# Kernel tuning notes

Measured on AMD Instinct MI355X. Metric: run time of the kernel, lower is better.

The kernel has to match this reference:

```python
import jax, jax.numpy as jnp
import numpy as np

B, S, D = 16, 2048, 1024   # batch, src_len, per-tensor feature dim (input_dim*growth_factor)
OUT = 1024                 # output_dim


def setup_inputs() -> dict:
    key = jax.random.key(0)
    k1, k2, k3, k4, k5, k6 = jax.random.split(key, 6)
    hidden = jax.random.normal(k1, (B, S, D), dtype=jnp.float32)
    encoder_outputs = jax.random.normal(k2, (B, S, D), dtype=jnp.float32)
    c_t = jax.random.normal(k3, (B, D), dtype=jnp.float32)
    # Linear(input_dim*3*growth_factor=3*D, OUT): PyTorch stores weight as [OUT, 3D]
    limit = 1.0 / np.sqrt(3 * D)
    W = jax.random.uniform(k4, (OUT, 3 * D), minval=-limit, maxval=limit, dtype=jnp.float32)
    b = jax.random.uniform(k5, (OUT,), minval=-limit, maxval=limit, dtype=jnp.float32)
    v = jax.random.uniform(k6, (OUT,), dtype=jnp.float32)  # torch.rand -> U[0,1)
    return {"hidden": hidden, "encoder_outputs": encoder_outputs, "c_t": c_t,
            "W": W, "b": b, "v": v}


def reference(hidden, encoder_outputs, c_t, W, b, v):
    # c_t broadcast over src_len; concat on feature dim -> [B, S, 3D]
    c_rep = jnp.broadcast_to(c_t[:, None, :], hidden.shape)
    cat = jnp.concatenate((hidden, c_rep, encoder_outputs), axis=2)
    # energy = relu(cat @ W^T + b): [B, S, OUT]
    energy = jax.nn.relu(jnp.einsum('bsf,of->bso', cat, W) + b)
    # attention = energy @ v: [B, S], then softmax over src_len
    attention = jnp.einsum('bso,o->bs', energy, v)
    return jax.nn.softmax(attention, axis=1)
```

## Files before the change

kernel.cpp:

```cpp
#include <hip/hip_runtime.h>
#include <hip/hip_bf16.h>


typedef __attribute__((ext_vector_type(8))) short short8;
typedef __attribute__((ext_vector_type(4))) float f32x4;
typedef __attribute__((ext_vector_type(8))) unsigned short ushort8v;
typedef __attribute__((ext_vector_type(4))) unsigned short ushort4v;

#define NB 16
#define NS 2048
#define ND 1024
#define NOUT 1024
#define NM (NB * NS)
#define KHE 2048
#define TM 256
#define TN 128
#define BK 64
#define NROWS (TM + TN)

#define PREP_ACONV 16384
#define PREP_WCONV 2048
#define PREP_CBIAS 256
#define PREP_ZERO 32

__device__ __forceinline__ unsigned short bf16_rne(float x) {
    unsigned int u = __float_as_uint(x);
    unsigned int r = (u + 0x7fffu + ((u >> 16) & 1u)) >> 16;
    return (unsigned short)r;
}

__device__ __forceinline__ void gload_lds16(const unsigned short* g, unsigned short* l) {
    __builtin_amdgcn_global_load_lds(
        (const __attribute__((address_space(1))) void*)g,
        (__attribute__((address_space(3))) void*)l, 16, 0, 0);
}

__global__ __launch_bounds__(256) void prep_k(const float* __restrict__ hidden,
                                              const float* __restrict__ enc,
                                              const float* __restrict__ c_t,
                                              const float* __restrict__ W,
                                              const float* __restrict__ bias,
                                              unsigned short* __restrict__ Abf,
                                              unsigned short* __restrict__ Wbf,
                                              float* __restrict__ cbias,
                                              float* __restrict__ logits) {
    const int bid = blockIdx.x;
    const int tid = threadIdx.x;
    if (bid < PREP_ACONV) {
        size_t c = (size_t)bid * 256 + tid;
        size_t m = c >> 7;
        int k = (int)(c & 127) * 16;
        const float* src = (k < ND) ? (hidden + m * ND + k) : (enc + m * ND + (k - ND));
        float4 f0 = ((const float4*)src)[0];
        float4 f1 = ((const float4*)src)[1];
        float4 f2 = ((const float4*)src)[2];
        float4 f3 = ((const float4*)src)[3];
        ushort8v h0, h1;
        h0[0] = bf16_rne(f0.x); h0[1] = bf16_rne(f0.y); h0[2] = bf16_rne(f0.z); h0[3] = bf16_rne(f0.w);
        h0[4] = bf16_rne(f1.x); h0[5] = bf16_rne(f1.y); h0[6] = bf16_rne(f1.z); h0[7] = bf16_rne(f1.w);
        h1[0] = bf16_rne(f2.x); h1[1] = bf16_rne(f2.y); h1[2] = bf16_rne(f2.z); h1[3] = bf16_rne(f2.w);
        h1[4] = bf16_rne(f3.x); h1[5] = bf16_rne(f3.y); h1[6] = bf16_rne(f3.z); h1[7] = bf16_rne(f3.w);
        *(ushort8v*)(Abf + m * KHE + k) = h0;
        *(ushort8v*)(Abf + m * KHE + k + 8) = h1;
    } else if (bid < PREP_ACONV + PREP_WCONV) {
        int idx = (bid - PREP_ACONV) * 256 + tid;
        int o = idx >> 9;
        int k = (idx & 511) * 4;
        int off = (k < ND) ? k : (k + ND);
        float4 f = *(const float4*)(W + (size_t)o * 3072 + off);
        ushort4v h;
        h.x = bf16_rne(f.x); h.y = bf16_rne(f.y); h.z = bf16_rne(f.z); h.w = bf16_rne(f.w);
        *(ushort4v*)(Wbf + (size_t)o * KHE + k) = h;
    } else if (bid < PREP_ACONV + PREP_WCONV + PREP_CBIAS) {
        int o = (bid - PREP_ACONV - PREP_WCONV) * 4 + (tid >> 6);
        int lane = tid & 63;
        const float* w = W + (size_t)o * 3072 + ND;
        float wr[16];
        #pragma unroll
        for (int j = 0; j < 16; ++j) wr[j] = w[lane + j * 64];
        float bo = bias[o];
        for (int b = 0; b < NB; ++b) {
            const float* cc = c_t + (size_t)b * ND;
            float s = 0.f;
            #pragma unroll
            for (int j = 0; j < 16; ++j) s = fmaf(cc[lane + j * 64], wr[j], s);
            #pragma unroll
            for (int m = 1; m < 64; m <<= 1) s += __shfl_xor(s, m);
            if (lane == 0) cbias[b * NOUT + o] = s + bo;
        }
    } else {
        int idx = (bid - PREP_ACONV - PREP_WCONV - PREP_CBIAS) * 256 + tid;
        ((float4*)logits)[idx] = make_float4(0.f, 0.f, 0.f, 0.f);
    }
}

__global__ __launch_bounds__(256) void wconv_k(const float* __restrict__ W,
                                               unsigned short* __restrict__ Wbf) {
    int idx = blockIdx.x * 256 + threadIdx.x;
    int o = idx >> 9;
    int k = (idx & 511) * 4;
    int off = (k < ND) ? k : (k + ND);
    float4 f = *(const float4*)(W + (size_t)o * 3072 + off);
    ushort4v h;
    h.x = bf16_rne(f.x); h.y = bf16_rne(f.y); h.z = bf16_rne(f.z); h.w = bf16_rne(f.w);
    *(ushort4v*)(Wbf + (size_t)o * KHE + k) = h;
}

__global__ __launch_bounds__(256) void cbias_k(const float* __restrict__ c_t,
                                               const float* __restrict__ W,
                                               const float* __restrict__ bias,
                                               float* __restrict__ cbias) {
    int o = blockIdx.x * 4 + (threadIdx.x >> 6);
    int lane = threadIdx.x & 63;
    const float* w = W + (size_t)o * 3072 + ND;
    float wr[16];
    #pragma unroll
    for (int j = 0; j < 16; ++j) wr[j] = w[lane + j * 64];
    float bo = bias[o];
    for (int b = 0; b < NB; ++b) {
        const float* c = c_t + (size_t)b * ND;
        float s = 0.f;
        #pragma unroll
        for (int j = 0; j < 16; ++j) s = fmaf(c[lane + j * 64], wr[j], s);
        #pragma unroll
        for (int m = 1; m < 64; m <<= 1) s += __shfl_xor(s, m);
        if (lane == 0) cbias[b * NOUT + o] = s + bo;
    }
}

__global__ __launch_bounds__(512, 4) void gemm_att_bf_k(const unsigned short* __restrict__ Abf,
                                                        const unsigned short* __restrict__ Wbf,
                                                        const float* __restrict__ cbias,
                                                        const float* __restrict__ v,
                                                        float* __restrict__ logits) {
    __shared__ unsigned short Ls[NROWS * BK] __attribute__((aligned(16)));
    __shared__ float rowsum[2][TM];
    __shared__ float cb_s[TN];
    __shared__ float v_s[TN];

    const int tid = threadIdx.x;
    const int bid = blockIdx.x;
    const int ntile = bid & 7;
    const int mtile = bid >> 3;
    const int m0 = mtile * TM;
    const int o0 = ntile * TN;
    const int batch = m0 >> 11;

    if (tid < TN) {
        cb_s[tid] = cbias[batch * NOUT + o0 + tid];
        v_s[tid] = v[o0 + tid];
    }

    const int wid = tid >> 6;
    const int lane = tid & 63;
    const int wm = (wid & 3) * 64;
    const int wn = (wid >> 2) * 64;

    const int srow = lane >> 3;
    const int schunk = (lane & 7) ^ srow;

    f32x4 acc[4][4] = {};

    for (int kt = 0; kt < KHE; kt += BK) {
        #pragma unroll
        for (int t = 0; t < 6; ++t) {
            const int r0 = wid * 48 + t * 8;
            const unsigned short* src = (r0 < TM)
                ? (Abf + (size_t)(m0 + r0 + srow) * KHE + kt + schunk * 8)
                : (Wbf + (size_t)(o0 + r0 - TM + srow) * KHE + kt + schunk * 8);
            gload_lds16(src, Ls + r0 * BK);
        }
        __syncthreads();

        #pragma unroll
        for (int s = 0; s < 2; ++s) {
            const int cbase = s * 4 + (lane >> 4);
            short8 a_frag[4], b_frag[4];
            #pragma unroll
            for (int i = 0; i < 4; ++i) {
                int row = wm + i * 16 + (lane & 15);
                a_frag[i] = *(const short8*)(Ls + row * BK + ((cbase ^ (row & 7)) * 8));
            }
            #pragma unroll
            for (int j = 0; j < 4; ++j) {
                int row = TM + wn + j * 16 + (lane & 15);
                b_frag[j] = *(const short8*)(Ls + row * BK + ((cbase ^ (row & 7)) * 8));
            }
            #pragma unroll
            for (int i = 0; i < 4; ++i)
                #pragma unroll
                for (int j = 0; j < 4; ++j)
                    acc[i][j] = __builtin_amdgcn_mfma_f32_16x16x32_bf16(a_frag[i], b_frag[j],
                                                                        acc[i][j], 0, 0, 0);
        }
        __syncthreads();
    }

    const int col = lane & 15;
    const int q = lane >> 4;
    float vv[4], cbv[4];
    #pragma unroll
    for (int j = 0; j < 4; ++j) {
        int oc = wn + j * 16 + col;
        vv[j] = v_s[oc];
        cbv[j] = cb_s[oc];
    }
    #pragma unroll
    for (int i = 0; i < 4; ++i) {
        #pragma unroll
        for (int r = 0; r < 4; ++r) {
            float s = 0.f;
            #pragma unroll
            for (int j = 0; j < 4; ++j) {
                float e = acc[i][j][r] + cbv[j];
                e = fmaxf(e, 0.f);
                s = fmaf(e, vv[j], s);
            }
            s += __shfl_xor(s, 1);
            s += __shfl_xor(s, 2);
            s += __shfl_xor(s, 4);
            s += __shfl_xor(s, 8);
            if (col == 0) rowsum[wid >> 2][wm + i * 16 + q * 4 + r] = s;
        }
    }
    __syncthreads();
    if (tid < TM) atomicAdd(&logits[m0 + tid], rowsum[0][tid] + rowsum[1][tid]);
}

__global__ __launch_bounds__(256) void gemm_att_k(const float* __restrict__ hidden,
                                                  const float* __restrict__ enc,
                                                  const unsigned short* __restrict__ Wbf,
                                                  const float* __restrict__ Wf,
                                                  const float* __restrict__ cbias,
                                                  const float* __restrict__ v,
                                                  float* __restrict__ logits,
                                                  int use_wbf) {
    __shared__ unsigned short As[128 * 32] __attribute__((aligned(16)));
    __shared__ unsigned short Bs[128 * 32] __attribute__((aligned(16)));
    __shared__ float rowsum[2][128];
    __shared__ float cb_s[128];
    __shared__ float v_s[128];

    const int tid = threadIdx.x;
    const int ntile = blockIdx.x & 7;
    const int mtile = blockIdx.x >> 3;
    const int m0 = mtile * 128;
    const int o0 = ntile * 128;
    const int batch = m0 >> 11;

    if (tid < 128) {
        cb_s[tid] = cbias[batch * NOUT + o0 + tid];
        v_s[tid] = v[o0 + tid];
    }

    const int wid = tid >> 6;
    const int lane = tid & 63;
    const int wm = (wid & 1) * 64;
    const int wn = (wid >> 1) * 64;

    f32x4 acc[4][4] = {};

    for (int kt = 0; kt < KHE; kt += 32) {
        const float* Abase = (kt < ND) ? hidden : enc;
        const int aoff = (kt < ND) ? kt : (kt - ND);
        #pragma unroll
        for (int i = 0; i < 4; ++i) {
            int p = tid + i * 256;
            int row = p >> 3, kc = p & 7;
            float4 f = *(const float4*)(Abase + (size_t)(m0 + row) * ND + aoff + kc * 4);
            ushort4v h;
            h.x = bf16_rne(f.x); h.y = bf16_rne(f.y); h.z = bf16_rne(f.z); h.w = bf16_rne(f.w);
            *(ushort4v*)(As + row * 32 + kc * 4) = h;
        }
        if (use_wbf) {
            #pragma unroll
            for (int i = 0; i < 2; ++i) {
                int u = tid + i * 256;
                int ol = u >> 2, kc = u & 3;
                ushort8v w8 = *(const ushort8v*)(Wbf + (size_t)(o0 + ol) * KHE + kt + kc * 8);
                *(ushort8v*)(Bs + ol * 32 + kc * 8) = w8;
            }
        } else {
            const int woff = (kt < ND) ? kt : (kt + ND);
            #pragma unroll
            for (int i = 0; i < 4; ++i) {
                int p = tid + i * 256;
                int row = p >> 3, kc = p & 7;
                float4 f = *(const float4*)(Wf + (size_t)(o0 + row) * 3072 + woff + kc * 4);
                ushort4v h;
                h.x = bf16_rne(f.x); h.y = bf16_rne(f.y); h.z = bf16_rne(f.z); h.w = bf16_rne(f.w);
                *(ushort4v*)(Bs + row * 32 + kc * 4) = h;
            }
        }
        __syncthreads();

        short8 a_frag[4], b_frag[4];
        #pragma unroll
        for (int i = 0; i < 4; ++i)
            a_frag[i] = *(const short8*)(As + (wm + i * 16 + (lane & 15)) * 32 + (lane >> 4) * 8);
        #pragma unroll
        for (int j = 0; j < 4; ++j)
            b_frag[j] = *(const short8*)(Bs + (wn + j * 16 + (lane & 15)) * 32 + (lane >> 4) * 8);
        #pragma unroll
        for (int i = 0; i < 4; ++i)
            #pragma unroll
            for (int j = 0; j < 4; ++j)
                acc[i][j] = __builtin_amdgcn_mfma_f32_16x16x32_bf16(a_frag[i], b_frag[j],
                                                                    acc[i][j], 0, 0, 0);
        __syncthreads();
    }

    const int col = lane & 15;
    const int q = lane >> 4;
    float vv[4], cbv[4];
    #pragma unroll
    for (int j = 0; j < 4; ++j) {
        int oc = wn + j * 16 + col;
        vv[j] = v_s[oc];
        cbv[j] = cb_s[oc];
    }
    #pragma unroll
    for (int i = 0; i < 4; ++i) {
        #pragma unroll
        for (int r = 0; r < 4; ++r) {
            float s = 0.f;
            #pragma unroll
            for (int j = 0; j < 4; ++j) {
                float e = acc[i][j][r] + cbv[j];
                e = fmaxf(e, 0.f);
                s = fmaf(e, vv[j], s);
            }
            s += __shfl_xor(s, 1);
            s += __shfl_xor(s, 2);
            s += __shfl_xor(s, 4);
            s += __shfl_xor(s, 8);
            if (col == 0) rowsum[wid >> 1][wm + i * 16 + q * 4 + r] = s;
        }
    }
    __syncthreads();
    if (tid < 128) atomicAdd(&logits[m0 + tid], rowsum[0][tid] + rowsum[1][tid]);
}

__global__ __launch_bounds__(256) void softmax_k(const float* __restrict__ logits,
                                                 float* __restrict__ out) {
    const int b = blockIdx.x;
    const int tid = threadIdx.x;
    const int lane = tid & 63, wid = tid >> 6;
    __shared__ float redmax[4];
    __shared__ float redsum[4];
    const float* L = logits + (size_t)b * NS;
    float x[8];
    float mx = -3.4e38f;
    #pragma unroll
    for (int i = 0; i < 8; ++i) {
        x[i] = L[tid + i * 256];
        mx = fmaxf(mx, x[i]);
    }
    #pragma unroll
    for (int m = 1; m < 64; m <<= 1) mx = fmaxf(mx, __shfl_xor(mx, m));
    if (lane == 0) redmax[wid] = mx;
    __syncthreads();
    mx = fmaxf(fmaxf(redmax[0], redmax[1]), fmaxf(redmax[2], redmax[3]));
    float sum = 0.f;
    #pragma unroll
    for (int i = 0; i < 8; ++i) {
        x[i] = expf(x[i] - mx);
        sum += x[i];
    }
    #pragma unroll
    for (int m = 1; m < 64; m <<= 1) sum += __shfl_xor(sum, m);
    if (lane == 0) redsum[wid] = sum;
    __syncthreads();
    float inv = 1.0f / (redsum[0] + redsum[1] + redsum[2] + redsum[3]);
    #pragma unroll
    for (int i = 0; i < 8; ++i) out[(size_t)b * NS + tid + i * 256] = x[i] * inv;
}

extern "C" void kernel_launch(void* const* d_in, const int* in_sizes, int n_in,
                              void* d_out, int out_size, void* d_ws, size_t ws_size,
                              hipStream_t stream) {
    const float* hidden = (const float*)d_in[0];
    const float* enc    = (const float*)d_in[1];
    const float* c_t    = (const float*)d_in[2];
    const float* W      = (const float*)d_in[3];
    const float* bias   = (const float*)d_in[4];
    const float* v      = (const float*)d_in[5];
    float* out = (float*)d_out;

    char* ws = (char*)d_ws;
    float* logits = (float*)ws;
    float* cbias  = (float*)(ws + 131072);
    unsigned short* Wbf = (unsigned short*)(ws + 196608);
    unsigned short* Abf = (unsigned short*)(ws + 196608 + 4194304);
    const size_t need_wbf = 196608 + (size_t)NOUT * KHE * 2;
    const size_t need_abf = need_wbf + (size_t)NM * KHE * 2;

    if (ws_size >= need_abf) {
        prep_k<<<PREP_ACONV + PREP_WCONV + PREP_CBIAS + PREP_ZERO, 256, 0, stream>>>(
            hidden, enc, c_t, W, bias, Abf, Wbf, cbias, logits);
        gemm_att_bf_k<<<(NM / TM) * (NOUT / TN), 512, 0, stream>>>(Abf, Wbf, cbias, v, logits);
    } else if (ws_size >= need_wbf) {
        hipMemsetAsync(logits, 0, NM * sizeof(float), stream);
        cbias_k<<<NOUT / 4, 256, 0, stream>>>(c_t, W, bias, cbias);
        wconv_k<<<(NOUT * KHE / 4) / 256, 256, 0, stream>>>(W, Wbf);
        gemm_att_k<<<(NM / 128) * (NOUT / 128), 256, 0, stream>>>(hidden, enc, Wbf, W, cbias, v,
                                                                  logits, 1);
    } else {
        hipMemsetAsync(logits, 0, NM * sizeof(float), stream);
        cbias_k<<<NOUT / 4, 256, 0, stream>>>(c_t, W, bias, cbias);
        gemm_att_k<<<(NM / 128) * (NOUT / 128), 256, 0, stream>>>(hidden, enc, Wbf, W, cbias, v,
                                                                  logits, 0);
    }
    softmax_k<<<NB, 256, 0, stream>>>(logits, out);
}
```

Before: 457.2 us.

## Fuse bf16 conversion, GEMM-attention and softmax into one persistent kernel

Replaces the prep kernel, the GEMM kernel and the softmax kernel with a single 512-block kernel. Each block converts its own slice of A to bf16, and the first 64 blocks also convert W and compute the context bias. Blocks then spin on global atomic counters before running two N-tiles of the MFMA GEMM, and the first 16 blocks wait for all blocks to finish before computing the softmax. This removes launch gaps and lets conversion overlap with compute. The cost is inter-block spin waits that assume all 512 blocks are co-resident, which risks deadlock if they are not, plus a reduced grid with more serial work per block.

```diff
diff --git a/kernel.cpp b/kernel.cpp
--- a/kernel.cpp
+++ b/kernel.cpp
@@ -18,11 +18,6 @@
 #define BK 64
 #define NROWS (TM + TN)
 
-#define PREP_ACONV 16384
-#define PREP_WCONV 2048
-#define PREP_CBIAS 256
-#define PREP_ZERO 32
-
 __device__ __forceinline__ unsigned short bf16_rne(float x) {
     unsigned int u = __float_as_uint(x);
     unsigned int r = (u + 0x7fffu + ((u >> 16) & 1u)) >> 16;
@@ -35,63 +30,232 @@
         (__attribute__((address_space(3))) void*)l, 16, 0, 0);
 }
 
-__global__ __launch_bounds__(256) void prep_k(const float* __restrict__ hidden,
-                                              const float* __restrict__ enc,
-                                              const float* __restrict__ c_t,
-                                              const float* __restrict__ W,
-                                              const float* __restrict__ bias,
-                                              unsigned short* __restrict__ Abf,
-                                              unsigned short* __restrict__ Wbf,
-                                              float* __restrict__ cbias,
-                                              float* __restrict__ logits) {
+__device__ __forceinline__ void cvt16(const float* src, unsigned short* dst) {
+    float4 f0 = ((const float4*)src)[0];
+    float4 f1 = ((const float4*)src)[1];
+    float4 f2 = ((const float4*)src)[2];
+    float4 f3 = ((const float4*)src)[3];
+    ushort8v h0, h1;
+    h0[0] = bf16_rne(f0.x); h0[1] = bf16_rne(f0.y); h0[2] = bf16_rne(f0.z); h0[3] = bf16_rne(f0.w);
+    h0[4] = bf16_rne(f1.x); h0[5] = bf16_rne(f1.y); h0[6] = bf16_rne(f1.z); h0[7] = bf16_rne(f1.w);
+    h1[0] = bf16_rne(f2.x); h1[1] = bf16_rne(f2.y); h1[2] = bf16_rne(f2.z); h1[3] = bf16_rne(f2.w);
+    h1[4] = bf16_rne(f3.x); h1[5] = bf16_rne(f3.y); h1[6] = bf16_rne(f3.z); h1[7] = bf16_rne(f3.w);
+    *(ushort8v*)dst = h0;
+    *(ushort8v*)(dst + 8) = h1;
+}
+
+__global__ __launch_bounds__(512, 4) void fused_k(const float* __restrict__ hidden,
+                                                  const float* __restrict__ enc,
+                                                  const float* __restrict__ c_t,
+                                                  const float* __restrict__ W,
+                                                  const float* __restrict__ bias,
+                                                  const float* __restrict__ v,
+                                                  unsigned int* __restrict__ ctr,
+                                                  unsigned short* __restrict__ Abf,
+                                                  unsigned short* __restrict__ Wbf,
+                                                  float* __restrict__ cbias,
+                                                  float* __restrict__ logits,
+                                                  float* __restrict__ out) {
+    __shared__ unsigned short Ls[NROWS * BK] __attribute__((aligned(16)));
+    __shared__ float rowsum[2][TM];
+    __shared__ float cb_s[TN];
+    __shared__ float v_s[TN];
+
+    const int tid = threadIdx.x;
     const int bid = blockIdx.x;
-    const int tid = threadIdx.x;
-    if (bid < PREP_ACONV) {
-        size_t c = (size_t)bid * 256 + tid;
-        size_t m = c >> 7;
-        int k = (int)(c & 127) * 16;
-        const float* src = (k < ND) ? (hidden + m * ND + k) : (enc + m * ND + (k - ND));
-        float4 f0 = ((const float4*)src)[0];
-        float4 f1 = ((const float4*)src)[1];
-        float4 f2 = ((const float4*)src)[2];
-        float4 f3 = ((const float4*)src)[3];
-        ushort8v h0, h1;
-        h0[0] = bf16_rne(f0.x); h0[1] = bf16_rne(f0.y); h0[2] = bf16_rne(f0.z); h0[3] = bf16_rne(f0.w);
-        h0[4] = bf16_rne(f1.x); h0[5] = bf16_rne(f1.y); h0[6] = bf16_rne(f1.z); h0[7] = bf16_rne(f1.w);
-        h1[0] = bf16_rne(f2.x); h1[1] = bf16_rne(f2.y); h1[2] = bf16_rne(f2.z); h1[3] = bf16_rne(f2.w);
-        h1[4] = bf16_rne(f3.x); h1[5] = bf16_rne(f3.y); h1[6] = bf16_rne(f3.z); h1[7] = bf16_rne(f3.w);
-        *(ushort8v*)(Abf + m * KHE + k) = h0;
-        *(ushort8v*)(Abf + m * KHE + k + 8) = h1;
-    } else if (bid < PREP_ACONV + PREP_WCONV) {
-        int idx = (bid - PREP_ACONV) * 256 + tid;
-        int o = idx >> 9;
-        int k = (idx & 511) * 4;
-        int off = (k < ND) ? k : (k + ND);
-        float4 f = *(const float4*)(W + (size_t)o * 3072 + off);
-        ushort4v h;
-        h.x = bf16_rne(f.x); h.y = bf16_rne(f.y); h.z = bf16_rne(f.z); h.w = bf16_rne(f.w);
-        *(ushort4v*)(Wbf + (size_t)o * KHE + k) = h;
-    } else if (bid < PREP_ACONV + PREP_WCONV + PREP_CBIAS) {
-        int o = (bid - PREP_ACONV - PREP_WCONV) * 4 + (tid >> 6);
-        int lane = tid & 63;
-        const float* w = W + (size_t)o * 3072 + ND;
-        float wr[16];
-        #pragma unroll
-        for (int j = 0; j < 16; ++j) wr[j] = w[lane + j * 64];
-        float bo = bias[o];
-        for (int b = 0; b < NB; ++b) {
-            const float* cc = c_t + (size_t)b * ND;
-            float s = 0.f;
-            #pragma unroll
-            for (int j = 0; j < 16; ++j) s = fmaf(cc[lane + j * 64], wr[j], s);
-            #pragma unroll
-            for (int m = 1; m < 64; m <<= 1) s += __shfl_xor(s, m);
-            if (lane == 0) cbias[b * NOUT + o] = s + bo;
-        }
-    } else {
-        int idx = (bid - PREP_ACONV - PREP_WCONV - PREP_CBIAS) * 256 + tid;
-        ((float4*)logits)[idx] = make_float4(0.f, 0.f, 0.f, 0.f);
-    }
+    const int mt = bid >> 2;
+    const int sub = bid & 3;
+
+    if (bid < 64) {
+        #pragma unroll
+        for (int c = 0; c < 4; ++c) {
+            int idx = tid + c * 512;
+            int o = bid * 16 + (idx >> 7);
+            int k = (idx & 127) * 16;
+            int off = (k < ND) ? k : (k + ND);
+            cvt16(W + (size_t)o * 3072 + off, Wbf + (size_t)o * KHE + k);
+        }
+        const int wv = tid >> 6, lane = tid & 63;
+        #pragma unroll
+        for (int u = 0; u < 2; ++u) {
+            int o = bid * 16 + wv * 2 + u;
+            const float* wrow = W + (size_t)o * 3072 + ND;
+            float wr[16];
+            #pragma unroll
+            for (int j = 0; j < 16; ++j) wr[j] = wrow[lane + j * 64];
+            float bo = bias[o];
+            for (int b = 0; b < NB; ++b) {
+                const float* cc = c_t + (size_t)b * ND;
+                float s = 0.f;
+                #pragma unroll
+                for (int j = 0; j < 16; ++j) s = fmaf(cc[lane + j * 64], wr[j], s);
+                #pragma unroll
+                for (int m = 1; m < 64; m <<= 1) s += __shfl_xor(s, m);
+                if (lane == 0) cbias[b * NOUT + o] = s + bo;
+            }
+        }
+        __syncthreads();
+        __threadfence();
+        if (tid == 0)
+            __hip_atomic_fetch_add(&ctr[0], 1u, __ATOMIC_RELEASE, __HIP_MEMORY_SCOPE_AGENT);
+    }
+
+    {
+        const float* base = (sub < 2) ? hidden : enc;
+        const int k0 = (sub & 1) * 512;
+        const int kd = sub * 512;
+        #pragma unroll
+        for (int c = 0; c < 16; ++c) {
+            int idx = tid + c * 512;
+            int r = idx >> 5;
+            int kc = (idx & 31) * 16;
+            cvt16(base + (size_t)(mt * 256 + r) * ND + k0 + kc,
+                  Abf + (size_t)(mt * 256 + r) * KHE + kd + kc);
+        }
+        __syncthreads();
+        __threadfence();
+        if (tid == 0)
+            __hip_atomic_fetch_add(&ctr[2 + mt], 1u, __ATOMIC_RELEASE, __HIP_MEMORY_SCOPE_AGENT);
+    }
+
+    if (tid == 0) {
+        while (__hip_atomic_load(&ctr[0], __ATOMIC_ACQUIRE, __HIP_MEMORY_SCOPE_AGENT) < 64u)
+            __builtin_amdgcn_s_sleep(16);
+        while (__hip_atomic_load(&ctr[2 + mt], __ATOMIC_ACQUIRE, __HIP_MEMORY_SCOPE_AGENT) < 4u)
+            __builtin_amdgcn_s_sleep(16);
+    }
+    __syncthreads();
+    __threadfence();
+
+    const int m0 = mt * TM;
+    const int batch = m0 >> 11;
+    const int wid = tid >> 6;
+    const int lane = tid & 63;
+    const int wm = (wid & 3) * 64;
+    const int wn = (wid >> 2) * 64;
+    const int srow = lane >> 3;
+    const int schunk = (lane & 7) ^ srow;
+
+    for (int t = 0; t < 2; ++t) {
+        const int o0 = (sub * 2 + t) * TN;
+        if (tid < TN) {
+            cb_s[tid] = cbias[batch * NOUT + o0 + tid];
+            v_s[tid] = v[o0 + tid];
+        }
+        f32x4 acc[4][4] = {};
+
+        for (int kt = 0; kt < KHE; kt += BK) {
+            #pragma unroll
+            for (int q = 0; q < 6; ++q) {
+                const int r0 = wid * 48 + q * 8;
+                const unsigned short* src = (r0 < TM)
+                    ? (Abf + (size_t)(m0 + r0 + srow) * KHE + kt + schunk * 8)
+                    : (Wbf + (size_t)(o0 + r0 - TM + srow) * KHE + kt + schunk * 8);
+                gload_lds16(src, Ls + r0 * BK);
+            }
+            __syncthreads();
+
+            #pragma unroll
+            for (int s = 0; s < 2; ++s) {
+                const int cbase = s * 4 + (lane >> 4);
+                short8 a_frag[4], b_frag[4];
+                #pragma unroll
+                for (int i = 0; i < 4; ++i) {
+                    int row = wm + i * 16 + (lane & 15);
+                    a_frag[i] = *(const short8*)(Ls + row * BK + ((cbase ^ (row & 7)) * 8));
+                }
+                #pragma unroll
+                for (int j = 0; j < 4; ++j) {
+                    int row = TM + wn + j * 16 + (lane & 15);
+                    b_frag[j] = *(const short8*)(Ls + row * BK + ((cbase ^ (row & 7)) * 8));
+                }
+                #pragma unroll
+                for (int i = 0; i < 4; ++i)
+                    #pragma unroll
+                    for (int j = 0; j < 4; ++j)
+                        acc[i][j] = __builtin_amdgcn_mfma_f32_16x16x32_bf16(a_frag[i], b_frag[j],
+                                                                            acc[i][j], 0, 0, 0);
+            }
+            __syncthreads();
+        }
+
+        const int col = lane & 15;
+        const int qq = lane >> 4;
+        float vv[4], cbv[4];
+        #pragma unroll
+        for (int j = 0; j < 4; ++j) {
+            int oc = wn + j * 16 + col;
+            vv[j] = v_s[oc];
+            cbv[j] = cb_s[oc];
+        }
+        #pragma unroll
+        for (int i = 0; i < 4; ++i) {
+            #pragma unroll
+            for (int r = 0; r < 4; ++r) {
+                float s = 0.f;
+                #pragma unroll
+                for (int j = 0; j < 4; ++j) {
+                    float e = acc[i][j][r] + cbv[j];
+                    e = fmaxf(e, 0.f);
+                    s = fmaf(e, vv[j], s);
+                }
+                s += __shfl_xor(s, 1);
+                s += __shfl_xor(s, 2);
+                s += __shfl_xor(s, 4);
+                s += __shfl_xor(s, 8);
+                if (col == 0) rowsum[wid >> 2][wm + i * 16 + qq * 4 + r] = s;
+            }
+        }
+        __syncthreads();
+        if (tid < TM) atomicAdd(&logits[m0 + tid], rowsum[0][tid] + rowsum[1][tid]);
+    }
+
+    __threadfence();
+    __syncthreads();
+    if (tid == 0)
+        __hip_atomic_fetch_add(&ctr[1], 1u, __ATOMIC_RELEASE, __HIP_MEMORY_SCOPE_AGENT);
+    if (bid >= 16) return;
+
+    if (tid == 0) {
+        while (__hip_atomic_load(&ctr[1], __ATOMIC_ACQUIRE, __HIP_MEMORY_SCOPE_AGENT) < 512u)
+            __builtin_amdgcn_s_sleep(16);
+    }
+    __syncthreads();
+    __threadfence();
+
+    const int wv = tid >> 6, ln = tid & 63;
+    float* red = rowsum[0];
+    const float* L = logits + (size_t)bid * NS;
+    float x[4];
+    float mx = -3.4e38f;
+    #pragma unroll
+    for (int i = 0; i < 4; ++i) {
+        x[i] = L[tid + i * 512];
+        mx = fmaxf(mx, x[i]);
+    }
+    #pragma unroll
+    for (int m = 1; m < 64; m <<= 1) mx = fmaxf(mx, __shfl_xor(mx, m));
+    if (ln == 0) red[wv] = mx;
+    __syncthreads();
+    mx = red[0];
+    #pragma unroll
+    for (int w = 1; w < 8; ++w) mx = fmaxf(mx, red[w]);
+    float sum = 0.f;
+    #pragma unroll
+    for (int i = 0; i < 4; ++i) {
+        x[i] = expf(x[i] - mx);
+        sum += x[i];
+    }
+    #pragma unroll
+    for (int m = 1; m < 64; m <<= 1) sum += __shfl_xor(sum, m);
+    if (ln == 0) red[8 + wv] = sum;
+    __syncthreads();
+    sum = 0.f;
+    #pragma unroll
+    for (int w = 0; w < 8; ++w) sum += red[8 + w];
+    float inv = 1.0f / sum;
+    #pragma unroll
+    for (int i = 0; i < 4; ++i) out[(size_t)bid * NS + tid + i * 512] = x[i] * inv;
 }
 
 __global__ __launch_bounds__(256) void wconv_k(const float* __restrict__ W,
@@ -126,105 +290,6 @@
         for (int m = 1; m < 64; m <<= 1) s += __shfl_xor(s, m);
         if (lane == 0) cbias[b * NOUT + o] = s + bo;
     }
-}
-
-__global__ __launch_bounds__(512, 4) void gemm_att_bf_k(const unsigned short* __restrict__ Abf,
-                                                        const unsigned short* __restrict__ Wbf,
-                                                        const float* __restrict__ cbias,
-                                                        const float* __restrict__ v,
-                                                        float* __restrict__ logits) {
-    __shared__ unsigned short Ls[NROWS * BK] __attribute__((aligned(16)));
-    __shared__ float rowsum[2][TM];
-    __shared__ float cb_s[TN];
-    __shared__ float v_s[TN];
-
-    const int tid = threadIdx.x;
-    const int bid = blockIdx.x;
-    const int ntile = bid & 7;
-    const int mtile = bid >> 3;
-    const int m0 = mtile * TM;
-    const int o0 = ntile * TN;
-    const int batch = m0 >> 11;
-
-    if (tid < TN) {
-        cb_s[tid] = cbias[batch * NOUT + o0 + tid];
-        v_s[tid] = v[o0 + tid];
-    }
-
-    const int wid = tid >> 6;
-    const int lane = tid & 63;
-    const int wm = (wid & 3) * 64;
-    const int wn = (wid >> 2) * 64;
-
-    const int srow = lane >> 3;
-    const int schunk = (lane & 7) ^ srow;
-
-    f32x4 acc[4][4] = {};
-
-    for (int kt = 0; kt < KHE; kt += BK) {
-        #pragma unroll
-        for (int t = 0; t < 6; ++t) {
-            const int r0 = wid * 48 + t * 8;
-            const unsigned short* src = (r0 < TM)
-                ? (Abf + (size_t)(m0 + r0 + srow) * KHE + kt + schunk * 8)
-                : (Wbf + (size_t)(o0 + r0 - TM + srow) * KHE + kt + schunk * 8);
-            gload_lds16(src, Ls + r0 * BK);
-        }
-        __syncthreads();
-
-        #pragma unroll
-        for (int s = 0; s < 2; ++s) {
-            const int cbase = s * 4 + (lane >> 4);
-            short8 a_frag[4], b_frag[4];
-            #pragma unroll
-            for (int i = 0; i < 4; ++i) {
-                int row = wm + i * 16 + (lane & 15);
-                a_frag[i] = *(const short8*)(Ls + row * BK + ((cbase ^ (row & 7)) * 8));
-            }
-            #pragma unroll
-            for (int j = 0; j < 4; ++j) {
-                int row = TM + wn + j * 16 + (lane & 15);
-                b_frag[j] = *(const short8*)(Ls + row * BK + ((cbase ^ (row & 7)) * 8));
-            }
-            #pragma unroll
-            for (int i = 0; i < 4; ++i)
-                #pragma unroll
-                for (int j = 0; j < 4; ++j)
-                    acc[i][j] = __builtin_amdgcn_mfma_f32_16x16x32_bf16(a_frag[i], b_frag[j],
-                                                                        acc[i][j], 0, 0, 0);
-        }
-        __syncthreads();
-    }
-
-    const int col = lane & 15;
-    const int q = lane >> 4;
-    float vv[4], cbv[4];
-    #pragma unroll
-    for (int j = 0; j < 4; ++j) {
-        int oc = wn + j * 16 + col;
-        vv[j] = v_s[oc];
-        cbv[j] = cb_s[oc];
-    }
-    #pragma unroll
-    for (int i = 0; i < 4; ++i) {
-        #pragma unroll
-        for (int r = 0; r < 4; ++r) {
-            float s = 0.f;
-            #pragma unroll
-            for (int j = 0; j < 4; ++j) {
-                float e = acc[i][j][r] + cbv[j];
-                e = fmaxf(e, 0.f);
-                s = fmaf(e, vv[j], s);
-            }
-            s += __shfl_xor(s, 1);
-            s += __shfl_xor(s, 2);
-            s += __shfl_xor(s, 4);
-            s += __shfl_xor(s, 8);
-            if (col == 0) rowsum[wid >> 2][wm + i * 16 + q * 4 + r] = s;
-        }
-    }
-    __syncthreads();
-    if (tid < TM) atomicAdd(&logits[m0 + tid], rowsum[0][tid] + rowsum[1][tid]);
 }
 
 __global__ __launch_bounds__(256) void gemm_att_k(const float* __restrict__ hidden,
@@ -388,28 +453,30 @@
     float* out = (float*)d_out;
 
     char* ws = (char*)d_ws;
-    float* logits = (float*)ws;
-    float* cbias  = (float*)(ws + 131072);
-    unsigned short* Wbf = (unsigned short*)(ws + 196608);
-    unsigned short* Abf = (unsigned short*)(ws + 196608 + 4194304);
-    const size_t need_wbf = 196608 + (size_t)NOUT * KHE * 2;
+    unsigned int* ctr = (unsigned int*)ws;
+    float* logits = (float*)(ws + 4096);
+    float* cbias  = (float*)(ws + 4096 + 131072);
+    unsigned short* Wbf = (unsigned short*)(ws + 4096 + 196608);
+    unsigned short* Abf = (unsigned short*)(ws + 4096 + 196608 + 4194304);
+    const size_t need_wbf = 4096 + 196608 + (size_t)NOUT * KHE * 2;
     const size_t need_abf = need_wbf + (size_t)NM * KHE * 2;
 
     if (ws_size >= need_abf) {
-        prep_k<<<PREP_ACONV + PREP_WCONV + PREP_CBIAS + PREP_ZERO, 256, 0, stream>>>(
-            hidden, enc, c_t, W, bias, Abf, Wbf, cbias, logits);
-        gemm_att_bf_k<<<(NM / TM) * (NOUT / TN), 512, 0, stream>>>(Abf, Wbf, cbias, v, logits);
+        hipMemsetAsync(ws, 0, 4096 + 131072, stream);
+        fused_k<<<512, 512, 0, stream>>>(hidden, enc, c_t, W, bias, v,
+                                         ctr, Abf, Wbf, cbias, logits, out);
     } else if (ws_size >= need_wbf) {
         hipMemsetAsync(logits, 0, NM * sizeof(float), stream);
         cbias_k<<<NOUT / 4, 256, 0, stream>>>(c_t, W, bias, cbias);
         wconv_k<<<(NOUT * KHE / 4) / 256, 256, 0, stream>>>(W, Wbf);
         gemm_att_k<<<(NM / 128) * (NOUT / 128), 256, 0, stream>>>(hidden, enc, Wbf, W, cbias, v,
                                                                   logits, 1);
+        softmax_k<<<NB, 256, 0, stream>>>(logits, out);
     } else {
         hipMemsetAsync(logits, 0, NM * sizeof(float), stream);
         cbias_k<<<NOUT / 4, 256, 0, stream>>>(c_t, W, bias, cbias);
         gemm_att_k<<<(NM / 128) * (NOUT / 128), 256, 0, stream>>>(hidden, enc, Wbf, W, cbias, v,
                                                                   logits, 0);
-    }
-    softmax_k<<<NB, 256, 0, stream>>>(logits, out);
-}
+        softmax_k<<<NB, 256, 0, stream>>>(logits, out);
+    }
+}
```

Measured after the change: 1.089 ms. 2.38x slower.
